# Performance work log

Hardware: AMD Instinct MI355X
Metric: run time of the kernel (lower is better)

The kernel has to match this reference:

```python
import jax, jax.numpy as jnp
import numpy as np
from itertools import product

N = 65536
G = 128          # voxel grid side
K = 27           # 3^3 kernel offsets
C_IN, C_HID, C_OUT = 3, 256, 128
EPS = 1e-5


def _build_neighbors():
    rng = np.random.default_rng(0)
    keys = np.sort(rng.choice(G ** 3, size=N, replace=False))
    coords = np.stack(np.unravel_index(keys, (G, G, G)), axis=-1)  # [N,3]
    offs = np.array(list(product([-1, 0, 1], repeat=3)), dtype=np.int64)  # [27,3]
    nc = coords[:, None, :] + offs[None, :, :]                       # [N,27,3]
    inb = ((nc >= 0) & (nc < G)).all(-1)
    nk = nc[..., 0] * G * G + nc[..., 1] * G + nc[..., 2]
    pos = np.clip(np.searchsorted(keys, np.clip(nk, 0, G ** 3 - 1)), 0, N - 1)
    found = inb & (keys[pos] == nk)
    idx = np.where(found, pos, 0).astype(np.int32)
    return idx, found


def setup_inputs() -> dict:
    key = jax.random.key(0)
    ks = jax.random.split(key, 12)
    idx, mask = _build_neighbors()
    s_in = 1.0 / np.sqrt(K * C_IN)
    s_h = 1.0 / np.sqrt(K * C_HID)
    return {
        "feats": jax.random.normal(ks[0], (N, C_IN), jnp.float32),
        "w_in": jax.random.normal(ks[1], (K, C_IN, C_HID), jnp.float32) * s_in,
        "g_in": jnp.ones((C_HID,), jnp.float32),
        "b_in": jnp.zeros((C_HID,), jnp.float32),
        "w_res": jax.random.normal(ks[2], (4, 2, K, C_HID, C_HID), jnp.float32) * s_h,
        "g_res": jnp.ones((4, 2, C_HID), jnp.float32),
        "b_res": jnp.zeros((4, 2, C_HID), jnp.float32),
        "w_out": jax.random.normal(ks[3], (C_HID, C_OUT), jnp.float32) / np.sqrt(C_HID),
        "nbr_idx": jnp.asarray(idx),
        "nbr_mask": jnp.asarray(mask),
    }


def sparse_conv(feats, W, idx, mask):
    # feats [N,Cin], W [K,Cin,Cout], idx/mask [N,K] -> gather-GEMM-scatter per offset
    def step(acc, xs):
        w_k, i_k, m_k = xs  # [Cin,Cout], [N], [N]
        g = feats[i_k] * m_k[:, None]
        return acc + g @ w_k, None
    init = jnp.zeros((feats.shape[0], W.shape[-1]), feats.dtype)
    out, _ = jax.lax.scan(step, init, (W, idx.T, mask.T.astype(feats.dtype)))
    return out


def bn(x, g, b):
    mu = x.mean(0)
    var = x.var(0)
    return (x - mu) * jax.lax.rsqrt(var + EPS) * g + b


def reference(feats, w_in, g_in, b_in, w_res, g_res, b_res, w_out, nbr_idx, nbr_mask):
    h = jax.nn.relu(bn(sparse_conv(feats, w_in, nbr_idx, nbr_mask), g_in, b_in))
    for i in range(4):  # 4 MinkowskiResBlocks
        r = jax.nn.relu(bn(sparse_conv(h, w_res[i, 0], nbr_idx, nbr_mask), g_res[i, 0], b_res[i, 0]))
        r = bn(sparse_conv(r, w_res[i, 1], nbr_idx, nbr_mask), g_res[i, 1], b_res[i, 1])
        h = jax.nn.relu(r + h)
    return h @ w_out  # kernel_size=1 output conv == pointwise linear
```

## Files before the change

kernel.cpp:

```cpp
#include <hip/hip_runtime.h>
#include <hip/hip_bf16.h>


#define NPTS 65536
#define CHID 256
#define CAP  4096
#define LBLK 256

typedef __bf16 bf16x8 __attribute__((ext_vector_type(8)));
typedef float  f32x4  __attribute__((ext_vector_type(4)));

__device__ __forceinline__ float bf2f(unsigned short u) {
    union { float f; unsigned v; } x; x.v = ((unsigned)u) << 16; return x.f;
}
__device__ __forceinline__ unsigned short f2bf(float f) {
    union { float f; unsigned v; } x; x.f = f;
    unsigned r = x.v + 0x7fffu + ((x.v >> 16) & 1u);
    return (unsigned short)(r >> 16);
}

__device__ __forceinline__ void gload16(const void* g, void* l) {
    __builtin_amdgcn_global_load_lds(
        (const __attribute__((address_space(1))) void*)g,
        (__attribute__((address_space(3))) void*)l, 16, 0, 0);
}

__device__ __forceinline__ void atomic_pk_bf16(unsigned short* p, unsigned v) {
    asm volatile("global_atomic_pk_add_bf16 %0, %1, off" :: "v"(p), "v"(v) : "memory");
}

__device__ __forceinline__ bool mk(const void* mask, int mflag, size_t i) {
    if (mflag) return ((const unsigned char*)mask)[i] != 0;
    return ((const int*)mask)[i] != 0;
}

__global__ void detect_mask(const unsigned char* __restrict__ m, int* __restrict__ flag) {
    int t = blockIdx.x * 256 + threadIdx.x;
    int any = 0;
    for (int i = t; i < 262144; i += 64 * 256)
        if ((i & 3) && m[i]) any = 1;
    if (any) atomicOr(flag, 1);
}

__global__ void pack_w(const float* __restrict__ w, unsigned short* __restrict__ wp) {
    __shared__ float tile[64][65];
    int m   = blockIdx.x;
    int tci = (blockIdx.y >> 2) * 64;
    int tco = (blockIdx.y & 3) * 64;
    const float* src = w + (size_t)m * 65536;
    unsigned short* dst = wp + (size_t)m * 65536;
    int t = threadIdx.x, c = t & 63, rg = t >> 6;
    for (int r = rg; r < 64; r += 4)
        tile[r][c] = src[(size_t)(tci + r) * 256 + tco + c];
    __syncthreads();
    for (int r = rg; r < 64; r += 4)
        dst[(size_t)(tco + r) * 256 + tci + c] = f2bf(tile[c][r]);
}

__global__ void pack_wout(const float* __restrict__ w, unsigned short* __restrict__ wp) {
    __shared__ float tile[64][65];
    int tco = blockIdx.x * 64, tci = blockIdx.y * 64;
    int t = threadIdx.x, c = t & 63, rg = t >> 6;
    for (int r = rg; r < 64; r += 4)
        tile[r][c] = w[(size_t)(tci + r) * 128 + tco + c];
    __syncthreads();
    for (int r = rg; r < 64; r += 4)
        wp[(size_t)(tco + r) * 256 + tci + c] = f2bf(tile[c][r]);
}

__global__ void pack_win(const float* __restrict__ w, unsigned short* __restrict__ wp) {
    __shared__ float tile[64][65];
    int cot = blockIdx.x * 64, kkt = blockIdx.y * 64;
    int t = threadIdx.x, c = t & 63, rg = t >> 6;
    for (int r = rg; r < 64; r += 4) {
        int kk = kkt + r;
        tile[r][c] = (kk < 81) ? w[(size_t)kk * 256 + cot + c] : 0.f;
    }
    __syncthreads();
    for (int r = rg; r < 64; r += 4)
        wp[(size_t)(cot + r) * 128 + kkt + c] = f2bf(tile[c][r]);
}

__global__ void count_lists(const void* __restrict__ mask, const int* __restrict__ mflagp,
                            int* __restrict__ blkcnt ) {
    int mflag = *mflagp;
    int tid = threadIdx.x, lane = tid & 63;
    int n = blockIdx.x * 256 + tid;
    __shared__ int lc[26];
    if (tid < 26) lc[tid] = 0;
    __syncthreads();
    unsigned vb = 0;
    for (int k = 0; k < 27; ++k) {
        if (k == 13) continue;
        if (mk(mask, mflag, (size_t)n * 27 + k)) vb |= 1u << k;
    }
    for (int k26 = 0; k26 < 26; ++k26) {
        int k = (k26 < 13) ? k26 : k26 + 1;
        unsigned long long b = __ballot((vb >> k) & 1);
        if (lane == 0) atomicAdd(&lc[k26], __popcll(b));
    }
    __syncthreads();
    if (tid < 26) blkcnt[tid * LBLK + blockIdx.x] = lc[tid];
}

__global__ void scan_lists(const int* __restrict__ blkcnt, int* __restrict__ bases,
                           int* __restrict__ cnt) {
    int t = threadIdx.x;
    if (t < 26) {
        int s = 0;
        for (int b = 0; b < LBLK; ++b) {
            bases[t * LBLK + b] = s;
            s += blkcnt[t * LBLK + b];
        }
        cnt[t] = s;
    }
}

__global__ void fill_lists(const int* __restrict__ idx, const void* __restrict__ mask,
                           const int* __restrict__ mflagp, const int* __restrict__ bases,
                           int* __restrict__ srcL, int* __restrict__ dstL) {
    int mflag = *mflagp;
    int tid = threadIdx.x, lane = tid & 63, wave = tid >> 6;
    int n = blockIdx.x * 256 + tid;
    __shared__ int wcnt[4][26];
    unsigned vb = 0;
    for (int k = 0; k < 27; ++k) {
        if (k == 13) continue;
        if (mk(mask, mflag, (size_t)n * 27 + k)) vb |= 1u << k;
    }
    for (int k26 = 0; k26 < 26; ++k26) {
        int k = (k26 < 13) ? k26 : k26 + 1;
        unsigned long long b = __ballot((vb >> k) & 1);
        if (lane == 0) wcnt[wave][k26] = __popcll(b);
    }
    __syncthreads();
    for (int k26 = 0; k26 < 26; ++k26) {
        int k = (k26 < 13) ? k26 : k26 + 1;
        bool v = (vb >> k) & 1;
        unsigned long long b = __ballot(v);
        if (v) {
            int p = bases[k26 * LBLK + blockIdx.x] + __popcll(b & ((1ull << lane) - 1ull));
            for (int w = 0; w < wave; ++w) p += wcnt[w][k26];
            if (p < CAP) {
                srcL[k26 * CAP + p] = idx[(size_t)n * 27 + k];
                dstL[k26 * CAP + p] = n;
            }
        }
    }
}

__global__ __launch_bounds__(256, 2)
void convin_gemm(const float* __restrict__ feats, const unsigned short* __restrict__ win,
                 const int* __restrict__ idx, const void* __restrict__ mask,
                 const int* __restrict__ mflagp, unsigned short* __restrict__ yb) {
    __shared__ __align__(16) char A[16384];
    __shared__ __align__(16) char B[32768];
    const int mflag = *mflagp;
    const int tid = threadIdx.x, lane = tid & 63, wave = tid >> 6;
    const int m0 = blockIdx.x * 64;

    for (int i = 0; i < 4; ++i)
        *(f32x4*)&A[tid * 64 + i * 16] = f32x4{0.f, 0.f, 0.f, 0.f};
    __syncthreads();

    {
        int row = tid & 63, g = tid >> 6;
        int n = m0 + row;
        int swz = (row & 7) << 4;
        for (int k = g; k < 27; k += 4) {
            if (mk(mask, mflag, (size_t)n * 27 + k)) {
                int j = idx[(size_t)n * 27 + k];
                float f0 = feats[j * 3 + 0], f1 = feats[j * 3 + 1], f2 = feats[j * 3 + 2];
                int b0 = 2 * (3 * k + 0), b1 = b0 + 2, b2 = b0 + 4;
                *(unsigned short*)&A[row * 256 + (b0 ^ swz)] = f2bf(f0);
                *(unsigned short*)&A[row * 256 + (b1 ^ swz)] = f2bf(f1);
                *(unsigned short*)&A[row * 256 + (b2 ^ swz)] = f2bf(f2);
            }
        }
    }

    const char* wb = (const char*)win;
    f32x4 acc[4][4] = {};

    for (int ks = 0; ks < 2; ++ks) {
        __syncthreads();
        for (int i = 0; i < 8; ++i) {
            int chunk = wave * 8 + i;
            int o = chunk * 1024 + lane * 16;
            int corow = o >> 7;
            int inner = (o & 127) ^ ((corow & 7) << 4);
            gload16(wb + (size_t)corow * 256 + ks * 128 + inner, B + o);
        }
        __syncthreads();
        const int cw = wave * 64;
        for (int kk = 0; kk < 64; kk += 32) {
            int kl = kk + 8 * (lane >> 4);
            bf16x8 af[4], bfr[4];
            for (int mi = 0; mi < 4; ++mi) {
                int row = 16 * mi + (lane & 15);
                af[mi] = *(const bf16x8*)(A + row * 256 + ((ks * 128 + 2 * kl) ^ ((row & 7) << 4)));
            }
            for (int ni = 0; ni < 4; ++ni) {
                int corow = cw + 16 * ni + (lane & 15);
                bfr[ni] = *(const bf16x8*)(B + corow * 128 + ((2 * kl) ^ ((corow & 7) << 4)));
            }
            for (int mi = 0; mi < 4; ++mi)
                for (int ni = 0; ni < 4; ++ni)
                    acc[mi][ni] = __builtin_amdgcn_mfma_f32_16x16x32_bf16(af[mi], bfr[ni], acc[mi][ni], 0, 0, 0);
        }
    }

    const int cw = wave * 64;
    const int rq = 4 * (lane >> 4);
    const int colo = lane & 15;
    for (int mi = 0; mi < 4; ++mi)
        for (int ni = 0; ni < 4; ++ni) {
            int col = cw + 16 * ni + colo;
            for (int r = 0; r < 4; ++r) {
                float v = acc[mi][ni][r];
                float o = __shfl_xor(v, 1);
                if ((lane & 1) == 0) {
                    unsigned pk = (unsigned)f2bf(v) | ((unsigned)f2bf(o) << 16);
                    int row = m0 + 16 * mi + rq + r;
                    *(unsigned*)&yb[(size_t)row * CHID + col] = pk;
                }
            }
        }
}

template<bool GATHER>
__global__ __launch_bounds__(512, 1)
void conv_gemm(const unsigned short* __restrict__ hin,
               const unsigned short* __restrict__ Wp,
               unsigned short* __restrict__ yb,
               const int* __restrict__ cnt,
               const int* __restrict__ srcL,
               const int* __restrict__ dstL) {
    __shared__ __align__(16) char lds[131072];
    __shared__ int ids_src[256];
    __shared__ int ids_dst[256];
    const int tid  = threadIdx.x;
    const int lane = tid & 63;
    const int wave = tid >> 6;
    const int wm = wave >> 2;
    const int wn = wave & 3;

    int k27, m0 = 0;
    if (GATHER) {
        int k26 = blockIdx.x;
        k27 = (k26 < 13) ? k26 : k26 + 1;
        int tile = blockIdx.y;
        int c = min(cnt[k26], CAP);
        if (tile * 256 >= c) return;
        if (tid < 256) {
            int g = tile * 256 + tid;
            bool v = (g < c);
            ids_src[tid] = v ? srcL[k26 * CAP + g] : 0;
            ids_dst[tid] = v ? dstL[k26 * CAP + g] : -1;
        }
        __syncthreads();
    } else {
        k27 = 13;
        m0 = blockIdx.x * 256;
    }
    const char* hbase = (const char*)hin;
    const char* wbase = (const char*)(Wp + (size_t)k27 * (CHID * CHID));

    f32x4 acc[8][4] = {};

    auto STAGE = [&](int buf, int ks) {
        const int ci0 = ks * 64;
        char* dst = lds + buf * 65536;
        #pragma unroll
        for (int i = 0; i < 8; ++i) {
            int o = (wave * 8 + i) * 1024 + lane * 16;
            const char* src;
            if (o < 32768) {
                int row = o >> 7;
                int inner = (o & 127) ^ ((row & 7) << 4);
                int grow = GATHER ? ids_src[row] : (m0 + row);
                src = hbase + (size_t)grow * 512 + ci0 * 2 + inner;
            } else {
                int bo = o - 32768;
                int corow = bo >> 7;
                int inner = (bo & 127) ^ ((corow & 7) << 4);
                src = wbase + (size_t)corow * 512 + ci0 * 2 + inner;
            }
            gload16(src, dst + o);
        }
    };

    auto COMPUTE = [&](int buf) {
        const char* A = lds + buf * 65536;
        const char* B = A + 32768;
        #pragma unroll
        for (int kk = 0; kk < 64; kk += 32) {
            int kl = kk + 8 * (lane >> 4);
            bf16x8 af[8], bfr[4];
            #pragma unroll
            for (int mi = 0; mi < 8; ++mi) {
                int row = wm * 128 + 16 * mi + (lane & 15);
                af[mi] = *(const bf16x8*)(A + row * 128 + ((2 * kl) ^ ((row & 7) << 4)));
            }
            #pragma unroll
            for (int ni = 0; ni < 4; ++ni) {
                int corow = wn * 64 + 16 * ni + (lane & 15);
                bfr[ni] = *(const bf16x8*)(B + corow * 128 + ((2 * kl) ^ ((corow & 7) << 4)));
            }
            #pragma unroll
            for (int mi = 0; mi < 8; ++mi)
                #pragma unroll
                for (int ni = 0; ni < 4; ++ni)
                    acc[mi][ni] = __builtin_amdgcn_mfma_f32_16x16x32_bf16(af[mi], bfr[ni], acc[mi][ni], 0, 0, 0);
        }
    };

    STAGE(0, 0);
    __syncthreads();
    int cur = 0;
    #pragma unroll
    for (int ks = 0; ks < 4; ++ks) {
        if (ks < 3) STAGE(cur ^ 1, ks + 1);
        COMPUTE(cur);
        __syncthreads();
        cur ^= 1;
    }

    const int rq = 4 * (lane >> 4);
    const int colo = lane & 15;
    #pragma unroll
    for (int mi = 0; mi < 8; ++mi)
        #pragma unroll
        for (int ni = 0; ni < 4; ++ni) {
            int col = wn * 64 + 16 * ni + colo;
            #pragma unroll
            for (int r = 0; r < 4; ++r) {
                float v = acc[mi][ni][r];
                float o = __shfl_xor(v, 1);
                if ((lane & 1) == 0) {
                    unsigned pk = (unsigned)f2bf(v) | ((unsigned)f2bf(o) << 16);
                    int rl = wm * 128 + 16 * mi + rq + r;
                    if (!GATHER) {
                        *(unsigned*)&yb[(size_t)(m0 + rl) * CHID + col] = pk;
                    } else {
                        int dst = ids_dst[rl];
                        if (dst >= 0)
                            atomic_pk_bf16(&yb[(size_t)dst * CHID + col], pk);
                    }
                }
            }
        }
}

__global__ void bn_stats(const unsigned short* __restrict__ yb, float* __restrict__ st) {
    int t = threadIdx.x;
    int b = blockIdx.x;
    float s = 0.f, s2 = 0.f;
    size_t base = (size_t)b * 256 * CHID + t;
    for (int i = 0; i < 256; ++i) {
        float v = bf2f(yb[base + (size_t)i * CHID]);
        s += v; s2 += v * v;
    }
    unsafeAtomicAdd(&st[t], s);
    unsafeAtomicAdd(&st[256 + t], s2);
}

__global__ void bn_apply(const unsigned short* __restrict__ yb, const float* __restrict__ st,
                         const float* __restrict__ g, const float* __restrict__ b,
                         const unsigned short* __restrict__ res, unsigned short* __restrict__ hout) {
    int t = threadIdx.x;
    float mean = st[t] * (1.f / NPTS);
    float var  = st[256 + t] * (1.f / NPTS) - mean * mean;
    float rstd = rsqrtf(var + 1e-5f);
    float sc = rstd * g[t];
    float bi = b[t] - mean * sc;
    size_t row0 = (size_t)blockIdx.x * 32;
    for (int i = 0; i < 32; ++i) {
        size_t off = (row0 + i) * CHID + t;
        float v = bf2f(yb[off]) * sc + bi;
        if (res) v += bf2f(res[off]);
        v = fmaxf(v, 0.f);
        hout[off] = f2bf(v);
    }
}

__global__ __launch_bounds__(256, 2)
void gemm_out(const unsigned short* __restrict__ hin, const unsigned short* __restrict__ wop,
              float* __restrict__ out) {
    __shared__ __align__(16) char lds[16384 + 16384];
    const int tid = threadIdx.x, lane = tid & 63, wave = tid >> 6;
    const int m0 = blockIdx.x * 128;
    const char* hb = (const char*)hin;
    const char* wb = (const char*)wop;
    f32x4 acc[4][4] = {};
    for (int ks = 0; ks < 4; ++ks) {
        int ci0 = ks * 64;
        __syncthreads();
        for (int i = 0; i < 8; ++i) {
            int chunk = wave * 8 + i;
            int o = chunk * 1024 + lane * 16;
            const char* src;
            if (o < 16384) {
                int row = o >> 7;
                int k2 = (o & 127) ^ ((row & 7) << 4);
                src = hb + (size_t)(m0 + row) * 512 + ci0 * 2 + k2;
            } else {
                int bo = o - 16384;
                int corow = bo >> 7;
                int k2 = (bo & 127) ^ ((corow & 7) << 4);
                src = wb + (size_t)corow * 512 + ci0 * 2 + k2;
            }
            gload16(src, lds + chunk * 1024);
        }
        __syncthreads();
        const char* A = lds;
        const char* B = lds + 16384;
        const int wm = wave >> 1, wn = wave & 1;
        for (int kk = 0; kk < 64; kk += 32) {
            int kl = kk + 8 * (lane >> 4);
            bf16x8 af[4], bfr[4];
            for (int mi = 0; mi < 4; ++mi) {
                int row = 64 * wm + 16 * mi + (lane & 15);
                af[mi] = *(const bf16x8*)(A + row * 128 + ((2 * kl) ^ ((row & 7) << 4)));
            }
            for (int ni = 0; ni < 4; ++ni) {
                int corow = 64 * wn + 16 * ni + (lane & 15);
                bfr[ni] = *(const bf16x8*)(B + corow * 128 + ((2 * kl) ^ ((corow & 7) << 4)));
            }
            for (int mi = 0; mi < 4; ++mi)
                for (int ni = 0; ni < 4; ++ni)
                    acc[mi][ni] = __builtin_amdgcn_mfma_f32_16x16x32_bf16(af[mi], bfr[ni], acc[mi][ni], 0, 0, 0);
        }
    }
    const int wm = wave >> 1, wn = wave & 1;
    for (int mi = 0; mi < 4; ++mi)
        for (int ni = 0; ni < 4; ++ni) {
            int col = 64 * wn + 16 * ni + (lane & 15);
            for (int r = 0; r < 4; ++r) {
                int row = m0 + 64 * wm + 16 * mi + 4 * (lane >> 4) + r;
                out[(size_t)row * 128 + col] = acc[mi][ni][r];
            }
        }
}

static const size_t OFF_Y    = 0;
static const size_t OFF_HA   = OFF_Y   + (size_t)NPTS * CHID * 2;
static const size_t OFF_HR   = OFF_HA  + (size_t)NPTS * CHID * 2;
static const size_t OFF_WP   = OFF_HR  + (size_t)NPTS * CHID * 2;
static const size_t OFF_WOP  = OFF_WP  + (size_t)8 * 27 * 65536 * 2;
static const size_t OFF_WIN  = OFF_WOP + (size_t)128 * 256 * 2;
static const size_t OFF_ST   = OFF_WIN + (size_t)256 * 128 * 2;
static const size_t OFF_CNT  = OFF_ST  + 9 * 512 * 4;
static const size_t OFF_FLAG = OFF_CNT + 112;
static const size_t OFF_SRC  = OFF_CNT + 128;
static const size_t OFF_DST  = OFF_SRC + (size_t)26 * CAP * 4;
static const size_t OFF_BLK  = OFF_DST + (size_t)26 * CAP * 4;
static const size_t OFF_BAS  = OFF_BLK + (size_t)26 * LBLK * 4;

extern "C" void kernel_launch(void* const* d_in, const int* in_sizes, int n_in,
                              void* d_out, int out_size, void* d_ws, size_t ws_size,
                              hipStream_t stream) {
    const float* feats = (const float*)d_in[0];
    const float* w_in  = (const float*)d_in[1];
    const float* g_in  = (const float*)d_in[2];
    const float* b_in  = (const float*)d_in[3];
    const float* w_res = (const float*)d_in[4];
    const float* g_res = (const float*)d_in[5];
    const float* b_res = (const float*)d_in[6];
    const float* w_out = (const float*)d_in[7];
    const int*   nidx  = (const int*)d_in[8];
    const void*  nmask = (const void*)d_in[9];

    char* ws = (char*)d_ws;
    unsigned short* Yb   = (unsigned short*)(ws + OFF_Y);
    unsigned short* HA   = (unsigned short*)(ws + OFF_HA);
    unsigned short* HR   = (unsigned short*)(ws + OFF_HR);
    unsigned short* WP   = (unsigned short*)(ws + OFF_WP);
    unsigned short* WOP  = (unsigned short*)(ws + OFF_WOP);
    unsigned short* WIN  = (unsigned short*)(ws + OFF_WIN);
    float*          ST   = (float*)(ws + OFF_ST);
    int*            CNT  = (int*)(ws + OFF_CNT);
    int*            MFLG = (int*)(ws + OFF_FLAG);
    int*            SRCL = (int*)(ws + OFF_SRC);
    int*            DSTL = (int*)(ws + OFF_DST);
    int*            BLKC = (int*)(ws + OFF_BLK);
    int*            BASE = (int*)(ws + OFF_BAS);

    hipMemsetAsync(ws + OFF_ST, 0, 9 * 512 * 4 + 128, stream);

    detect_mask<<<64, 256, 0, stream>>>((const unsigned char*)nmask, MFLG);
    pack_w   <<<dim3(216, 16), 256, 0, stream>>>(w_res, WP);
    pack_wout<<<dim3(2, 4),    256, 0, stream>>>(w_out, WOP);
    pack_win <<<dim3(4, 2),    256, 0, stream>>>(w_in, WIN);

    count_lists<<<LBLK, 256, 0, stream>>>(nmask, MFLG, BLKC);
    scan_lists <<<1, 64, 0, stream>>>(BLKC, BASE, CNT);
    fill_lists <<<LBLK, 256, 0, stream>>>(nidx, nmask, MFLG, BASE, SRCL, DSTL);

    convin_gemm<<<NPTS / 64, 256, 0, stream>>>(feats, WIN, nidx, nmask, MFLG, Yb);
    bn_stats<<<256, 256, 0, stream>>>(Yb, ST);
    bn_apply<<<2048, 256, 0, stream>>>(Yb, ST, g_in, b_in, nullptr, HA);

    for (int c8 = 0; c8 < 8; ++c8) {
        const unsigned short* hin = (c8 & 1) ? HR : HA;
        const unsigned short* wbase = WP + (size_t)c8 * 27 * 65536;
        conv_gemm<false><<<NPTS / 256, 512, 0, stream>>>(hin, wbase, Yb, nullptr, nullptr, nullptr);
        conv_gemm<true><<<dim3(26, CAP / 256), 512, 0, stream>>>(hin, wbase, Yb, CNT, SRCL, DSTL);
        float* st = ST + (size_t)(1 + c8) * 512;
        bn_stats<<<256, 256, 0, stream>>>(Yb, st);
        if (c8 & 1) {
            bn_apply<<<2048, 256, 0, stream>>>(Yb, st, g_res + c8 * 256, b_res + c8 * 256, HA, HA);
        } else {
            bn_apply<<<2048, 256, 0, stream>>>(Yb, st, g_res + c8 * 256, b_res + c8 * 256, nullptr, HR);
        }
    }

    gemm_out<<<NPTS / 128, 256, 0, stream>>>(HA, WOP, (float*)d_out);
}
```

Measured before the change: 968.0 us.

## Replace bf16 atomic scatter with per-entry buffer and fused gather-combine plus BN stats

The gather GEMM used to scatter-add its results into the output rows with packed bf16 atomics. It now writes each entry's result densely to a staging buffer. A new combine kernel then sums, for each point, its centre result and its neighbour entries through a per-point entry list, and accumulates the batch-norm sums in the same pass, replacing the separate bn_stats kernel. This removes atomic contention and reduces bf16 rounding during accumulation, at the cost of an extra staging buffer (about 26*CAP rows) and an indirect gather in the combine kernel.

```diff
diff --git a/kernel.cpp b/kernel.cpp
--- a/kernel.cpp
+++ b/kernel.cpp
@@ -9,6 +9,7 @@
 
 typedef __bf16 bf16x8 __attribute__((ext_vector_type(8)));
 typedef float  f32x4  __attribute__((ext_vector_type(4)));
+typedef unsigned short u16x8 __attribute__((ext_vector_type(8)));
 
 __device__ __forceinline__ float bf2f(unsigned short u) {
     union { float f; unsigned v; } x; x.v = ((unsigned)u) << 16; return x.f;
@@ -23,10 +24,6 @@
     __builtin_amdgcn_global_load_lds(
         (const __attribute__((address_space(1))) void*)g,
         (__attribute__((address_space(3))) void*)l, 16, 0, 0);
-}
-
-__device__ __forceinline__ void atomic_pk_bf16(unsigned short* p, unsigned v) {
-    asm volatile("global_atomic_pk_add_bf16 %0, %1, off" :: "v"(p), "v"(v) : "memory");
 }
 
 __device__ __forceinline__ bool mk(const void* mask, int mflag, size_t i) {
@@ -118,7 +115,8 @@
 
 __global__ void fill_lists(const int* __restrict__ idx, const void* __restrict__ mask,
                            const int* __restrict__ mflagp, const int* __restrict__ bases,
-                           int* __restrict__ srcL, int* __restrict__ dstL) {
+                           int* __restrict__ srcL, int* __restrict__ nbrEnt,
+                           unsigned char* __restrict__ nbrCnt) {
     int mflag = *mflagp;
     int tid = threadIdx.x, lane = tid & 63, wave = tid >> 6;
     int n = blockIdx.x * 256 + tid;
@@ -134,6 +132,7 @@
         if (lane == 0) wcnt[wave][k26] = __popcll(b);
     }
     __syncthreads();
+    int j = 0;
     for (int k26 = 0; k26 < 26; ++k26) {
         int k = (k26 < 13) ? k26 : k26 + 1;
         bool v = (vb >> k) & 1;
@@ -143,10 +142,12 @@
             for (int w = 0; w < wave; ++w) p += wcnt[w][k26];
             if (p < CAP) {
                 srcL[k26 * CAP + p] = idx[(size_t)n * 27 + k];
-                dstL[k26 * CAP + p] = n;
-            }
-        }
-    }
+                nbrEnt[n * 32 + j] = k26 * CAP + p;
+                ++j;
+            }
+        }
+    }
+    nbrCnt[n] = (unsigned char)j;
 }
 
 __global__ __launch_bounds__(256, 2)
@@ -234,33 +235,28 @@
                const unsigned short* __restrict__ Wp,
                unsigned short* __restrict__ yb,
                const int* __restrict__ cnt,
-               const int* __restrict__ srcL,
-               const int* __restrict__ dstL) {
+               const int* __restrict__ srcL) {
     __shared__ __align__(16) char lds[131072];
     __shared__ int ids_src[256];
-    __shared__ int ids_dst[256];
     const int tid  = threadIdx.x;
     const int lane = tid & 63;
     const int wave = tid >> 6;
     const int wm = wave >> 2;
     const int wn = wave & 3;
 
-    int k27, m0 = 0;
+    int k27 = 13, m0 = 0, k26 = 0, tile = 0, c = 0;
     if (GATHER) {
-        int k26 = blockIdx.x;
+        k26 = blockIdx.x;
         k27 = (k26 < 13) ? k26 : k26 + 1;
-        int tile = blockIdx.y;
-        int c = min(cnt[k26], CAP);
+        tile = blockIdx.y;
+        c = min(cnt[k26], CAP);
         if (tile * 256 >= c) return;
         if (tid < 256) {
             int g = tile * 256 + tid;
-            bool v = (g < c);
-            ids_src[tid] = v ? srcL[k26 * CAP + g] : 0;
-            ids_dst[tid] = v ? dstL[k26 * CAP + g] : -1;
+            ids_src[tid] = (g < c) ? srcL[k26 * CAP + g] : 0;
         }
         __syncthreads();
     } else {
-        k27 = 13;
         m0 = blockIdx.x * 256;
     }
     const char* hbase = (const char*)hin;
@@ -343,13 +339,62 @@
                     if (!GATHER) {
                         *(unsigned*)&yb[(size_t)(m0 + rl) * CHID + col] = pk;
                     } else {
-                        int dst = ids_dst[rl];
-                        if (dst >= 0)
-                            atomic_pk_bf16(&yb[(size_t)dst * CHID + col], pk);
+                        int g = tile * 256 + rl;
+                        if (g < c)
+                            *(unsigned*)&yb[((size_t)k26 * CAP + g) * CHID + col] = pk;
                     }
                 }
             }
         }
+}
+
+__global__ __launch_bounds__(256)
+void combine_stats(unsigned short* __restrict__ Yb,
+                   const unsigned short* __restrict__ buf,
+                   const int* __restrict__ nbrEnt,
+                   const unsigned char* __restrict__ nbrCnt,
+                   float* __restrict__ st) {
+    __shared__ float ssum[8][256];
+    __shared__ float ssq[8][256];
+    const int tid = threadIdx.x;
+    const int grp = tid >> 5;
+    const int c0  = (tid & 31) * 8;
+    float s[8] = {}, s2[8] = {};
+    const int row0 = blockIdx.x * 128;
+    for (int it = 0; it < 16; ++it) {
+        int row = row0 + it * 8 + grp;
+        size_t off = (size_t)row * CHID + c0;
+        u16x8 y = *(const u16x8*)&Yb[off];
+        float v[8];
+        #pragma unroll
+        for (int q = 0; q < 8; ++q) v[q] = bf2f(y[q]);
+        int cnt = nbrCnt[row];
+        for (int j = 0; j < cnt; ++j) {
+            int e = nbrEnt[row * 32 + j];
+            u16x8 b = *(const u16x8*)&buf[(size_t)e * CHID + c0];
+            #pragma unroll
+            for (int q = 0; q < 8; ++q) v[q] += bf2f(b[q]);
+        }
+        u16x8 o;
+        #pragma unroll
+        for (int q = 0; q < 8; ++q) {
+            o[q] = f2bf(v[q]);
+            s[q] += v[q];
+            s2[q] += v[q] * v[q];
+        }
+        *(u16x8*)&Yb[off] = o;
+    }
+    #pragma unroll
+    for (int q = 0; q < 8; ++q) {
+        ssum[grp][c0 + q] = s[q];
+        ssq[grp][c0 + q]  = s2[q];
+    }
+    __syncthreads();
+    float ts = 0.f, tq = 0.f;
+    #pragma unroll
+    for (int g = 0; g < 8; ++g) { ts += ssum[g][tid]; tq += ssq[g][tid]; }
+    unsafeAtomicAdd(&st[tid], ts);
+    unsafeAtomicAdd(&st[256 + tid], tq);
 }
 
 __global__ void bn_stats(const unsigned short* __restrict__ yb, float* __restrict__ st) {
@@ -453,9 +498,11 @@
 static const size_t OFF_CNT  = OFF_ST  + 9 * 512 * 4;
 static const size_t OFF_FLAG = OFF_CNT + 112;
 static const size_t OFF_SRC  = OFF_CNT + 128;
-static const size_t OFF_DST  = OFF_SRC + (size_t)26 * CAP * 4;
-static const size_t OFF_BLK  = OFF_DST + (size_t)26 * CAP * 4;
+static const size_t OFF_BLK  = OFF_SRC + (size_t)26 * CAP * 4;
 static const size_t OFF_BAS  = OFF_BLK + (size_t)26 * LBLK * 4;
+static const size_t OFF_NBE  = OFF_BAS + (size_t)26 * LBLK * 4;
+static const size_t OFF_NBC  = OFF_NBE + (size_t)NPTS * 32 * 4;
+static const size_t OFF_BUF  = OFF_NBC + (size_t)NPTS;
 
 extern "C" void kernel_launch(void* const* d_in, const int* in_sizes, int n_in,
                               void* d_out, int out_size, void* d_ws, size_t ws_size,
@@ -482,9 +529,11 @@
     int*            CNT  = (int*)(ws + OFF_CNT);
     int*            MFLG = (int*)(ws + OFF_FLAG);
     int*            SRCL = (int*)(ws + OFF_SRC);
-    int*            DSTL = (int*)(ws + OFF_DST);
     int*            BLKC = (int*)(ws + OFF_BLK);
     int*            BASE = (int*)(ws + OFF_BAS);
+    int*            NBE  = (int*)(ws + OFF_NBE);
+    unsigned char*  NBC  = (unsigned char*)(ws + OFF_NBC);
+    unsigned short* BUF  = (unsigned short*)(ws + OFF_BUF);
 
     hipMemsetAsync(ws + OFF_ST, 0, 9 * 512 * 4 + 128, stream);
 
@@ -495,7 +544,7 @@
 
     count_lists<<<LBLK, 256, 0, stream>>>(nmask, MFLG, BLKC);
     scan_lists <<<1, 64, 0, stream>>>(BLKC, BASE, CNT);
-    fill_lists <<<LBLK, 256, 0, stream>>>(nidx, nmask, MFLG, BASE, SRCL, DSTL);
+    fill_lists <<<LBLK, 256, 0, stream>>>(nidx, nmask, MFLG, BASE, SRCL, NBE, NBC);
 
     convin_gemm<<<NPTS / 64, 256, 0, stream>>>(feats, WIN, nidx, nmask, MFLG, Yb);
     bn_stats<<<256, 256, 0, stream>>>(Yb, ST);
@@ -504,10 +553,10 @@
     for (int c8 = 0; c8 < 8; ++c8) {
         const unsigned short* hin = (c8 & 1) ? HR : HA;
         const unsigned short* wbase = WP + (size_t)c8 * 27 * 65536;
-        conv_gemm<false><<<NPTS / 256, 512, 0, stream>>>(hin, wbase, Yb, nullptr, nullptr, nullptr);
-        conv_gemm<true><<<dim3(26, CAP / 256), 512, 0, stream>>>(hin, wbase, Yb, CNT, SRCL, DSTL);
         float* st = ST + (size_t)(1 + c8) * 512;
-        bn_stats<<<256, 256, 0, stream>>>(Yb, st);
+        conv_gemm<false><<<NPTS / 256, 512, 0, stream>>>(hin, wbase, Yb, nullptr, nullptr);
+        conv_gemm<true><<<dim3(26, CAP / 256), 512, 0, stream>>>(hin, wbase, BUF, CNT, SRCL);
+        combine_stats<<<512, 256, 0, stream>>>(Yb, BUF, NBE, NBC, st);
         if (c8 & 1) {
             bn_apply<<<2048, 256, 0, stream>>>(Yb, st, g_res + c8 * 256, b_res + c8 * 256, HA, HA);
         } else {
```

After: 885.4 us. 1.09x faster.
